# Performance work log

Measured on AMD Instinct MI355X. Metric: run time of the kernel, lower is better.

The kernel has to match this reference:

```python
import jax, jax.numpy as jnp
import numpy as np

N_NODES = 100000
N_EDGES = 3200000
N_FEAT = 256
N_FILT = 256


def setup_inputs() -> dict:
    key = jax.random.key(0)
    k1, k2, k3, k4, k5 = jax.random.split(key, 5)
    # Xavier-normal-ish filters: std = sqrt(2/(fan_in+fan_out))
    std = (2.0 / (N_FEAT + N_FILT)) ** 0.5
    filters = jax.random.normal(k1, (N_FEAT, N_FILT), dtype=jnp.float32) * std
    x = jax.random.normal(k2, (N_NODES, N_FEAT), dtype=jnp.float32)
    edge_row = jax.random.randint(k3, (N_EDGES,), 0, N_NODES, dtype=jnp.int32)
    edge_col = jax.random.randint(k4, (N_EDGES,), 0, N_NODES, dtype=jnp.int32)
    edge_weight = jax.random.uniform(k5, (N_EDGES,), dtype=jnp.float32)
    return {"x": x, "filters": filters, "edge_row": edge_row,
            "edge_col": edge_col, "edge_weight": edge_weight}


def reference(x, filters, edge_row, edge_col, edge_weight):
    # XF = x @ filters  -> [N, K]
    XF = jnp.matmul(x, filters)
    # out = transform @ XF, transform given in COO form:
    # out[r] = sum_{e: row[e]==r} weight[e] * XF[col[e]]
    msgs = edge_weight[:, None] * XF[edge_col]          # [E, K] gather
    out = jax.ops.segment_sum(msgs, edge_row, num_segments=N_NODES)  # [N, K] scatter-add
    return out
```

## Files before the change

### kernel.cpp

```cpp
#include <hip/hip_runtime.h>

#define NF 256
#define NK 256
#define NBKT 512
#define TILEA 8192

typedef __attribute__((ext_vector_type(8))) short bf16x8;
typedef __attribute__((ext_vector_type(4))) float f32x4;

__device__ __forceinline__ ushort f2bf(float f) {
  uint u = __float_as_uint(f);
  return (ushort)((u + 0x7fffu + ((u >> 16) & 1u)) >> 16);
}
__device__ __forceinline__ float bf2f(ushort h) {
  return __uint_as_float(((uint)h) << 16);
}

__global__ __launch_bounds__(256) void prelude(const float* __restrict__ F,
                                               ushort* __restrict__ Ft,
                                               const int* __restrict__ erow,
                                               int* __restrict__ bcnt, int nE) {
  __shared__ int h[NBKT];
  if (blockIdx.x < NF) {
    int k = blockIdx.x;
    int n = threadIdx.x;
    Ft[(size_t)n * NF + k] = f2bf(F[(size_t)k * NK + n]);
    return;
  }
  const int bid = blockIdx.x - NF;
  const int nb = gridDim.x - NF;
  h[threadIdx.x] = 0;
  h[threadIdx.x + 256] = 0;
  __syncthreads();
  for (int e = bid * 256 + threadIdx.x; e < nE; e += nb * 256)
    atomicAdd(&h[erow[e] >> 8], 1);
  __syncthreads();
  int v0 = h[threadIdx.x], v1 = h[threadIdx.x + 256];
  if (v0) atomicAdd(&bcnt[threadIdx.x], v0);
  if (v1) atomicAdd(&bcnt[threadIdx.x + 256], v1);
}

__global__ __launch_bounds__(256) void gemm_mfma(const float* __restrict__ x,
                                                 const ushort* __restrict__ Ft,
                                                 ushort* __restrict__ XFh, int M) {
  __shared__ ushort As[32 * NF];
  const int t = threadIdx.x;
  const int row0 = blockIdx.x * 32;

  const float4* xv = (const float4*)(x + (size_t)row0 * NF);
#pragma unroll
  for (int j = 0; j < 8; ++j) {
    int idx = j * 256 + t;
    int r = idx >> 6;
    int c4 = idx & 63;
    float4 v = make_float4(0.f, 0.f, 0.f, 0.f);
    if (row0 + r < M) v = xv[idx];
    ushort4 hh = make_ushort4(f2bf(v.x), f2bf(v.y), f2bf(v.z), f2bf(v.w));
    uint boff = (uint)(r * 512 + c4 * 8);
    boff ^= (uint)((r & 7) << 4);
    *(ushort4*)((char*)As + boff) = hh;
  }
  __syncthreads();

  const int lane = t & 63;
  const int wv = t >> 6;
  const int arow = lane & 15;
  const int kg = lane >> 4;

  bf16x8 afr[2][8];
#pragma unroll
  for (int rt = 0; rt < 2; ++rt) {
#pragma unroll
    for (int kk = 0; kk < 8; ++kk) {
      int r = rt * 16 + arow;
      uint boff = (uint)(r * 512 + kk * 64 + kg * 16);
      boff ^= (uint)((r & 7) << 4);
      afr[rt][kk] = *(const bf16x8*)((const char*)As + boff);
    }
  }

  f32x4 acc[2][4];
#pragma unroll
  for (int rt = 0; rt < 2; ++rt)
#pragma unroll
    for (int f = 0; f < 4; ++f) acc[rt][f] = (f32x4){0.f, 0.f, 0.f, 0.f};

  const int ncol0 = wv * 64;
#pragma unroll
  for (int f = 0; f < 4; ++f) {
    const ushort* bp = Ft + (size_t)(ncol0 + f * 16 + arow) * NF + kg * 8;
#pragma unroll
    for (int kk = 0; kk < 8; ++kk) {
      bf16x8 bfr = *(const bf16x8*)(bp + kk * 32);
      acc[0][f] = __builtin_amdgcn_mfma_f32_16x16x32_bf16(afr[0][kk], bfr, acc[0][f], 0, 0, 0);
      acc[1][f] = __builtin_amdgcn_mfma_f32_16x16x32_bf16(afr[1][kk], bfr, acc[1][f], 0, 0, 0);
    }
  }

#pragma unroll
  for (int rt = 0; rt < 2; ++rt) {
#pragma unroll
    for (int f = 0; f < 4; ++f) {
      int col = ncol0 + f * 16 + arow;
#pragma unroll
      for (int rg = 0; rg < 4; ++rg) {
        int row = row0 + rt * 16 + kg * 4 + rg;
        if (row < M) XFh[(size_t)row * NK + col] = f2bf(acc[rt][f][rg]);
      }
    }
  }
}

__global__ __launch_bounds__(512) void scan_bbase(const int* __restrict__ bcnt,
                                                  int* __restrict__ bbase,
                                                  int* __restrict__ bcursor) {
  __shared__ int s[NBKT];
  int t = threadIdx.x;
  int v = bcnt[t];
  s[t] = v;
  __syncthreads();
  for (int d = 1; d < NBKT; d <<= 1) {
    int tmp = (t >= d) ? s[t - d] : 0;
    __syncthreads();
    s[t] += tmp;
    __syncthreads();
  }
  int excl = s[t] - v;
  bbase[t] = excl;
  bcursor[t * 16] = excl;
}

__global__ __launch_bounds__(512) void bin_coarse(const int* __restrict__ erow,
                                                  const int* __restrict__ ecol,
                                                  const float* __restrict__ ew,
                                                  int* __restrict__ bcursor,
                                                  int2* __restrict__ tmpCW, int nE) {
  __shared__ int h[NBKT];
  __shared__ int lb[NBKT];
  __shared__ int gb[NBKT];
  __shared__ int2 pay[TILEA];
  const int t = threadIdx.x;
  const int base = blockIdx.x * TILEA;

  h[t] = 0;
  __syncthreads();

  int rnk[16], bb[16], loc[16];
#pragma unroll
  for (int k = 0; k < 16; ++k) {
    int i = base + k * 512 + t;
    rnk[k] = -1; bb[k] = 0; loc[k] = 0;
    if (i < nE) {
      int row = erow[i];
      bb[k] = row >> 8;
      loc[k] = row & 255;
      rnk[k] = atomicAdd(&h[bb[k]], 1);
    }
  }
  __syncthreads();

  int hv = h[t];
  lb[t] = hv;
  __syncthreads();
  for (int d = 1; d < NBKT; d <<= 1) {
    int tmp = (t >= d) ? lb[t - d] : 0;
    __syncthreads();
    lb[t] += tmp;
    __syncthreads();
  }
  int ex = lb[t] - hv;
  __syncthreads();
  lb[t] = ex;
  if (hv > 0) gb[t] = atomicAdd(&bcursor[t * 16], hv);
  __syncthreads();

#pragma unroll
  for (int k = 0; k < 16; ++k) {
    int i = base + k * 512 + t;
    if (i < nE) {
      int pos = lb[bb[k]] + rnk[k];
      pay[pos] = make_int2(ecol[i] | (loc[k] << 20), __float_as_int(ew[i]));
    }
  }
  __syncthreads();

  const int wv = t >> 6, lane = t & 63;
  for (int b = wv; b < NBKT; b += 8) {
    int len = h[b];
    if (!len) continue;
    int lbase = lb[b], gbase = gb[b];
    for (int off = lane; off < len; off += 64)
      tmpCW[gbase + off] = pay[lbase + off];
  }
}

__global__ __launch_bounds__(256) void bin_fine(const int2* __restrict__ tmpCW,
                                                const int* __restrict__ bbase,
                                                const int* __restrict__ bcnt,
                                                int* __restrict__ offsets,
                                                int2* __restrict__ cw,
                                                int nNodes, int nE) {
  __shared__ int hist[256];
  __shared__ int cur[256];
  const int b = blockIdx.x;
  const int t = threadIdx.x;
  const int base = bbase[b];
  const int n = bcnt[b];

  hist[t] = 0;
  __syncthreads();
  for (int i = t; i < n; i += 256)
    atomicAdd(&hist[((uint)tmpCW[base + i].x) >> 20], 1);
  __syncthreads();

  int hv = hist[t];
  cur[t] = hv;
  __syncthreads();
  for (int d = 1; d < 256; d <<= 1) {
    int tmp = (t >= d) ? cur[t - d] : 0;
    __syncthreads();
    cur[t] += tmp;
    __syncthreads();
  }
  int ex = cur[t] - hv;
  __syncthreads();
  cur[t] = ex;
  int node = (b << 8) + t;
  if (node < nNodes) offsets[node] = base + ex;
  if (b == 0 && t == 0) offsets[nNodes] = nE;
  __syncthreads();

  for (int i = t; i < n; i += 256) {
    int2 v = tmpCW[base + i];
    int local = ((uint)v.x) >> 20;
    int d = base + atomicAdd(&cur[local], 1);
    cw[d] = make_int2(v.x & 0xFFFFF, v.y);
  }
}

__global__ __launch_bounds__(256) void gather_bf16(const ushort* __restrict__ XFh,
                                                   const int* __restrict__ offsets,
                                                   const int2* __restrict__ cw,
                                                   f32x4* __restrict__ outv,
                                                   int nNodes) {
  const int lane = threadIdx.x & 63;
  const int node = (blockIdx.x * blockDim.x + threadIdx.x) >> 6;
  if (node >= nNodes) return;
  const int start = offsets[node];
  const int end = offsets[node + 1];
  const ushort4* XV = (const ushort4*)XFh;

  float ax = 0.f, ay = 0.f, az = 0.f, aw = 0.f;
  for (int base = start; base < end; base += 64) {
    int n = end - base;
    if (n > 64) n = 64;
    int2 e = make_int2(0, 0);
    if (lane < n) {
      long long raw = __builtin_nontemporal_load((const long long*)(cw + base + lane));
      e.x = (int)(raw & 0xFFFFFFFFll);
      e.y = (int)(raw >> 32);
    }
    int j = 0;
    for (; j + 7 < n; j += 8) {
      int c0 = __shfl(e.x, j),     c1 = __shfl(e.x, j + 1);
      int c2 = __shfl(e.x, j + 2), c3 = __shfl(e.x, j + 3);
      int c4 = __shfl(e.x, j + 4), c5 = __shfl(e.x, j + 5);
      int c6 = __shfl(e.x, j + 6), c7 = __shfl(e.x, j + 7);
      float w0 = __int_as_float(__shfl(e.y, j));
      float w1 = __int_as_float(__shfl(e.y, j + 1));
      float w2 = __int_as_float(__shfl(e.y, j + 2));
      float w3 = __int_as_float(__shfl(e.y, j + 3));
      float w4 = __int_as_float(__shfl(e.y, j + 4));
      float w5 = __int_as_float(__shfl(e.y, j + 5));
      float w6 = __int_as_float(__shfl(e.y, j + 6));
      float w7 = __int_as_float(__shfl(e.y, j + 7));
      ushort4 v0 = XV[(size_t)c0 * 64 + lane];
      ushort4 v1 = XV[(size_t)c1 * 64 + lane];
      ushort4 v2 = XV[(size_t)c2 * 64 + lane];
      ushort4 v3 = XV[(size_t)c3 * 64 + lane];
      ushort4 v4 = XV[(size_t)c4 * 64 + lane];
      ushort4 v5 = XV[(size_t)c5 * 64 + lane];
      ushort4 v6 = XV[(size_t)c6 * 64 + lane];
      ushort4 v7 = XV[(size_t)c7 * 64 + lane];
      ax += w0 * bf2f(v0.x); ay += w0 * bf2f(v0.y); az += w0 * bf2f(v0.z); aw += w0 * bf2f(v0.w);
      ax += w1 * bf2f(v1.x); ay += w1 * bf2f(v1.y); az += w1 * bf2f(v1.z); aw += w1 * bf2f(v1.w);
      ax += w2 * bf2f(v2.x); ay += w2 * bf2f(v2.y); az += w2 * bf2f(v2.z); aw += w2 * bf2f(v2.w);
      ax += w3 * bf2f(v3.x); ay += w3 * bf2f(v3.y); az += w3 * bf2f(v3.z); aw += w3 * bf2f(v3.w);
      ax += w4 * bf2f(v4.x); ay += w4 * bf2f(v4.y); az += w4 * bf2f(v4.z); aw += w4 * bf2f(v4.w);
      ax += w5 * bf2f(v5.x); ay += w5 * bf2f(v5.y); az += w5 * bf2f(v5.z); aw += w5 * bf2f(v5.w);
      ax += w6 * bf2f(v6.x); ay += w6 * bf2f(v6.y); az += w6 * bf2f(v6.z); aw += w6 * bf2f(v6.w);
      ax += w7 * bf2f(v7.x); ay += w7 * bf2f(v7.y); az += w7 * bf2f(v7.z); aw += w7 * bf2f(v7.w);
    }
    for (; j + 3 < n; j += 4) {
      int c0 = __shfl(e.x, j),     c1 = __shfl(e.x, j + 1);
      int c2 = __shfl(e.x, j + 2), c3 = __shfl(e.x, j + 3);
      float w0 = __int_as_float(__shfl(e.y, j));
      float w1 = __int_as_float(__shfl(e.y, j + 1));
      float w2 = __int_as_float(__shfl(e.y, j + 2));
      float w3 = __int_as_float(__shfl(e.y, j + 3));
      ushort4 v0 = XV[(size_t)c0 * 64 + lane];
      ushort4 v1 = XV[(size_t)c1 * 64 + lane];
      ushort4 v2 = XV[(size_t)c2 * 64 + lane];
      ushort4 v3 = XV[(size_t)c3 * 64 + lane];
      ax += w0 * bf2f(v0.x); ay += w0 * bf2f(v0.y); az += w0 * bf2f(v0.z); aw += w0 * bf2f(v0.w);
      ax += w1 * bf2f(v1.x); ay += w1 * bf2f(v1.y); az += w1 * bf2f(v1.z); aw += w1 * bf2f(v1.w);
      ax += w2 * bf2f(v2.x); ay += w2 * bf2f(v2.y); az += w2 * bf2f(v2.z); aw += w2 * bf2f(v2.w);
      ax += w3 * bf2f(v3.x); ay += w3 * bf2f(v3.y); az += w3 * bf2f(v3.z); aw += w3 * bf2f(v3.w);
    }
    for (; j < n; ++j) {
      int c0 = __shfl(e.x, j);
      float w0 = __int_as_float(__shfl(e.y, j));
      ushort4 v0 = XV[(size_t)c0 * 64 + lane];
      ax += w0 * bf2f(v0.x); ay += w0 * bf2f(v0.y); az += w0 * bf2f(v0.z); aw += w0 * bf2f(v0.w);
    }
  }
  f32x4 r; r.x = ax; r.y = ay; r.z = az; r.w = aw;
  __builtin_nontemporal_store(r, &outv[(size_t)node * 64 + lane]);
}

__global__ __launch_bounds__(256) void gemm_xf(const float* __restrict__ x,
                                               const float* __restrict__ F,
                                               float* __restrict__ XF, int M) {
  __shared__ float xs[64][NF];
  const int t = threadIdx.x;
  const int row0 = blockIdx.x * 64;
  const int rows = min(64, M - row0);
  const float4* xv = (const float4*)(x + (size_t)row0 * NF);
  float4* xsv = (float4*)&xs[0][0];
#pragma unroll
  for (int j = 0; j < 16; ++j) {
    int i = j * 256 + t;
    int r = i >> 6;
    float4 v;
    if (r < rows) v = xv[i];
    else          v = make_float4(0.f, 0.f, 0.f, 0.f);
    xsv[i] = v;
  }
  __syncthreads();
  const int r0 = (t >> 5) * 8;
  const int c0 = blockIdx.y * 128 + (t & 31) * 4;
  float acc[8][4];
#pragma unroll
  for (int r = 0; r < 8; ++r)
#pragma unroll
    for (int c = 0; c < 4; ++c) acc[r][c] = 0.f;
  for (int k = 0; k < NF; k += 4) {
    float4 f0 = *(const float4*)(F + (size_t)(k + 0) * NK + c0);
    float4 f1 = *(const float4*)(F + (size_t)(k + 1) * NK + c0);
    float4 f2 = *(const float4*)(F + (size_t)(k + 2) * NK + c0);
    float4 f3 = *(const float4*)(F + (size_t)(k + 3) * NK + c0);
#pragma unroll
    for (int r = 0; r < 8; ++r) {
      float4 xr = *(const float4*)&xs[r0 + r][k];
      acc[r][0] += xr.x * f0.x + xr.y * f1.x + xr.z * f2.x + xr.w * f3.x;
      acc[r][1] += xr.x * f0.y + xr.y * f1.y + xr.z * f2.y + xr.w * f3.y;
      acc[r][2] += xr.x * f0.z + xr.y * f1.z + xr.z * f2.z + xr.w * f3.z;
      acc[r][3] += xr.x * f0.w + xr.y * f1.w + xr.z * f2.w + xr.w * f3.w;
    }
  }
#pragma unroll
  for (int r = 0; r < 8; ++r) {
    int row = r0 + r;
    if (row < rows) {
      float4 v = make_float4(acc[r][0], acc[r][1], acc[r][2], acc[r][3]);
      *(float4*)(XF + (size_t)(row0 + row) * NK + c0) = v;
    }
  }
}

__global__ __launch_bounds__(256) void scatter_edges(
    const float* __restrict__ XF, const int* __restrict__ erow,
    const int* __restrict__ ecol, const float* __restrict__ ew,
    float* __restrict__ out, int nE) {
  const int lane = threadIdx.x & 63;
  const int wid = (blockIdx.x * blockDim.x + threadIdx.x) >> 6;
  const int nwaves = (gridDim.x * blockDim.x) >> 6;
  for (int e = wid; e < nE; e += nwaves) {
    const int r = erow[e];
    const int c = ecol[e];
    const float w = ew[e];
    float4 v = *(const float4*)(XF + (size_t)c * NK + lane * 4);
    float* dst = out + (size_t)r * NK + lane * 4;
    atomicAdd(dst + 0, w * v.x);
    atomicAdd(dst + 1, w * v.y);
    atomicAdd(dst + 2, w * v.z);
    atomicAdd(dst + 3, w * v.w);
  }
}

static inline size_t align16(size_t x) { return (x + 15) & ~(size_t)15; }

extern "C" void kernel_launch(void* const* d_in, const int* in_sizes, int n_in,
                              void* d_out, int out_size, void* d_ws, size_t ws_size,
                              hipStream_t stream) {
  const float* x  = (const float*)d_in[0];
  const float* F  = (const float*)d_in[1];
  const int* erow = (const int*)d_in[2];
  const int* ecol = (const int*)d_in[3];
  const float* ew = (const float*)d_in[4];
  float* out      = (float*)d_out;

  const int M      = in_sizes[0] / NF;
  const int nE     = in_sizes[2];
  const int nNodes = out_size / NK;

  char* base = (char*)d_ws;
  size_t off = 0;
  ushort* XFh  = (ushort*)(base + off); off += align16((size_t)M * NK * sizeof(ushort));
  ushort* Ft   = (ushort*)(base + off); off += align16((size_t)NF * NK * sizeof(ushort));
  int* offsets = (int*)(base + off);    off += align16(((size_t)nNodes + 1) * sizeof(int));
  int* bcnt    = (int*)(base + off);    off += align16(NBKT * sizeof(int));
  int* bbase   = (int*)(base + off);    off += align16(NBKT * sizeof(int));
  int* bcursor = (int*)(base + off);    off += align16((size_t)NBKT * 16 * sizeof(int));
  int2* tmpCW  = (int2*)(base + off);   off += align16((size_t)nE * sizeof(int2));
  int2* cw     = (int2*)(base + off);   off += align16((size_t)nE * sizeof(int2));
  const size_t needed = off;

  const int nb2 = (nNodes + 255) >> 8;
  const bool ok = (ws_size >= needed) && (nb2 <= NBKT) &&
                  (nNodes < (1 << 20)) && (M < (1 << 20));

  if (ok) {
    hipMemsetAsync(bcnt, 0, NBKT * sizeof(int), stream);
    prelude<<<NF + 2048, 256, 0, stream>>>(F, Ft, erow, bcnt, nE);
    gemm_mfma<<<(M + 31) / 32, 256, 0, stream>>>(x, Ft, XFh, M);
    scan_bbase<<<1, NBKT, 0, stream>>>(bcnt, bbase, bcursor);
    bin_coarse<<<(nE + TILEA - 1) / TILEA, 512, 0, stream>>>(erow, ecol, ew,
                                                             bcursor, tmpCW, nE);
    bin_fine<<<nb2, 256, 0, stream>>>(tmpCW, bbase, bcnt, offsets, cw, nNodes, nE);
    int gblocks = (nNodes + 3) / 4;
    gather_bf16<<<gblocks, 256, 0, stream>>>(XFh, offsets, cw, (f32x4*)out, nNodes);
  } else {
    float* XF = (float*)d_ws;
    dim3 gg((M + 63) / 64, NK / 128);
    gemm_xf<<<gg, 256, 0, stream>>>(x, F, XF, M);
    hipMemsetAsync(d_out, 0, (size_t)out_size * sizeof(float), stream);
    scatter_edges<<<2048, 256, 0, stream>>>(XF, erow, ecol, ew, out, nE);
  }
}
```

Measured before the change: 432.5 us.

## Fuse fine binning and gather into one per-bucket LDS kernel

Shrinks coarse row buckets from 256 to 128 nodes, doubling the bucket count to 1024. Each block of the new kernel counting-sorts its bucket's edges into shared memory and then gathers and accumulates each node's output directly. This drops the global sorted-edge array and the offsets array, along with the extra write and read of all edges. In exchange the gather runs on far fewer waves, each with shallower load unrolling, and a bucket that overflows shared memory falls back to float atomics.

```diff
diff --git a/kernel.cpp b/kernel.cpp
--- a/kernel.cpp
+++ b/kernel.cpp
@@ -2,8 +2,11 @@
 
 #define NF 256
 #define NK 256
-#define NBKT 512
+#define BSHIFT 7
+#define NLOC 128
+#define NBKT 1024
 #define TILEA 8192
+#define GCAP 5120
 
 typedef __attribute__((ext_vector_type(8))) short bf16x8;
 typedef __attribute__((ext_vector_type(4))) float f32x4;
@@ -29,15 +32,17 @@
   }
   const int bid = blockIdx.x - NF;
   const int nb = gridDim.x - NF;
-  h[threadIdx.x] = 0;
-  h[threadIdx.x + 256] = 0;
+#pragma unroll
+  for (int j = 0; j < 4; ++j) h[threadIdx.x + j * 256] = 0;
   __syncthreads();
   for (int e = bid * 256 + threadIdx.x; e < nE; e += nb * 256)
-    atomicAdd(&h[erow[e] >> 8], 1);
-  __syncthreads();
-  int v0 = h[threadIdx.x], v1 = h[threadIdx.x + 256];
-  if (v0) atomicAdd(&bcnt[threadIdx.x], v0);
-  if (v1) atomicAdd(&bcnt[threadIdx.x + 256], v1);
+    atomicAdd(&h[erow[e] >> BSHIFT], 1);
+  __syncthreads();
+#pragma unroll
+  for (int j = 0; j < 4; ++j) {
+    int v = h[threadIdx.x + j * 256];
+    if (v) atomicAdd(&bcnt[threadIdx.x + j * 256], v);
+  }
 }
 
 __global__ __launch_bounds__(256) void gemm_mfma(const float* __restrict__ x,
@@ -111,9 +116,9 @@
   }
 }
 
-__global__ __launch_bounds__(512) void scan_bbase(const int* __restrict__ bcnt,
-                                                  int* __restrict__ bbase,
-                                                  int* __restrict__ bcursor) {
+__global__ __launch_bounds__(NBKT) void scan_bbase(const int* __restrict__ bcnt,
+                                                   int* __restrict__ bbase,
+                                                   int* __restrict__ bcursor) {
   __shared__ int s[NBKT];
   int t = threadIdx.x;
   int v = bcnt[t];
@@ -138,11 +143,12 @@
   __shared__ int h[NBKT];
   __shared__ int lb[NBKT];
   __shared__ int gb[NBKT];
+  __shared__ int ps[512];
   __shared__ int2 pay[TILEA];
   const int t = threadIdx.x;
   const int base = blockIdx.x * TILEA;
 
-  h[t] = 0;
+  h[t] = 0; h[t + 512] = 0;
   __syncthreads();
 
   int rnk[16], bb[16], loc[16];
@@ -152,26 +158,32 @@
     rnk[k] = -1; bb[k] = 0; loc[k] = 0;
     if (i < nE) {
       int row = erow[i];
-      bb[k] = row >> 8;
-      loc[k] = row & 255;
+      bb[k] = row >> BSHIFT;
+      loc[k] = row & (NLOC - 1);
       rnk[k] = atomicAdd(&h[bb[k]], 1);
     }
   }
   __syncthreads();
 
-  int hv = h[t];
-  lb[t] = hv;
-  __syncthreads();
-  for (int d = 1; d < NBKT; d <<= 1) {
-    int tmp = (t >= d) ? lb[t - d] : 0;
-    __syncthreads();
-    lb[t] += tmp;
-    __syncthreads();
-  }
-  int ex = lb[t] - hv;
-  __syncthreads();
-  lb[t] = ex;
-  if (hv > 0) gb[t] = atomicAdd(&bcursor[t * 16], hv);
+  int a0 = h[2 * t], a1 = h[2 * t + 1];
+  ps[t] = a0 + a1;
+  __syncthreads();
+  for (int d = 1; d < 512; d <<= 1) {
+    int tmp = (t >= d) ? ps[t - d] : 0;
+    __syncthreads();
+    ps[t] += tmp;
+    __syncthreads();
+  }
+  int pb = ps[t] - (a0 + a1);
+  lb[2 * t] = pb;
+  lb[2 * t + 1] = pb + a0;
+  __syncthreads();
+
+  {
+    int v0 = h[t], v1 = h[t + 512];
+    if (v0) gb[t] = atomicAdd(&bcursor[t * 16], v0);
+    if (v1) gb[t + 512] = atomicAdd(&bcursor[(t + 512) * 16], v1);
+  }
   __syncthreads();
 
 #pragma unroll
@@ -194,128 +206,100 @@
   }
 }
 
-__global__ __launch_bounds__(256) void bin_fine(const int2* __restrict__ tmpCW,
-                                                const int* __restrict__ bbase,
-                                                const int* __restrict__ bcnt,
-                                                int* __restrict__ offsets,
-                                                int2* __restrict__ cw,
-                                                int nNodes, int nE) {
-  __shared__ int hist[256];
-  __shared__ int cur[256];
+__global__ __launch_bounds__(512) void bucket_gather(const int2* __restrict__ tmpCW,
+                                                     const int* __restrict__ bbase,
+                                                     const int* __restrict__ bcnt,
+                                                     const ushort* __restrict__ XFh,
+                                                     f32x4* __restrict__ outv,
+                                                     float* __restrict__ outf,
+                                                     int nNodes) {
+  __shared__ int st[NLOC];
+  __shared__ int cur[NLOC];
+  __shared__ int2 pay[GCAP];
+  const int t = threadIdx.x;
   const int b = blockIdx.x;
-  const int t = threadIdx.x;
   const int base = bbase[b];
   const int n = bcnt[b];
-
-  hist[t] = 0;
-  __syncthreads();
-  for (int i = t; i < n; i += 256)
-    atomicAdd(&hist[((uint)tmpCW[base + i].x) >> 20], 1);
-  __syncthreads();
-
-  int hv = hist[t];
-  cur[t] = hv;
-  __syncthreads();
-  for (int d = 1; d < 256; d <<= 1) {
-    int tmp = (t >= d) ? cur[t - d] : 0;
-    __syncthreads();
-    cur[t] += tmp;
-    __syncthreads();
-  }
-  int ex = cur[t] - hv;
-  __syncthreads();
-  cur[t] = ex;
-  int node = (b << 8) + t;
-  if (node < nNodes) offsets[node] = base + ex;
-  if (b == 0 && t == 0) offsets[nNodes] = nE;
-  __syncthreads();
-
-  for (int i = t; i < n; i += 256) {
+  const int nl = (n < GCAP) ? n : GCAP;
+  const ushort4* XV = (const ushort4*)XFh;
+
+  if (t < NLOC) cur[t] = 0;
+  __syncthreads();
+  for (int i = t; i < nl; i += 512)
+    atomicAdd(&cur[((uint)tmpCW[base + i].x) >> 20], 1);
+  __syncthreads();
+
+  int hv = (t < NLOC) ? cur[t] : 0;
+  if (t < NLOC) st[t] = hv;
+  __syncthreads();
+  for (int d = 1; d < NLOC; d <<= 1) {
+    int tmp = (t >= d && t < NLOC) ? st[t - d] : 0;
+    __syncthreads();
+    if (t < NLOC) st[t] += tmp;
+    __syncthreads();
+  }
+  if (t < NLOC) {
+    st[t] -= hv;
+    cur[t] = st[t];
+  }
+  __syncthreads();
+
+  for (int i = t; i < nl; i += 512) {
     int2 v = tmpCW[base + i];
-    int local = ((uint)v.x) >> 20;
-    int d = base + atomicAdd(&cur[local], 1);
-    cw[d] = make_int2(v.x & 0xFFFFF, v.y);
-  }
-}
-
-__global__ __launch_bounds__(256) void gather_bf16(const ushort* __restrict__ XFh,
-                                                   const int* __restrict__ offsets,
-                                                   const int2* __restrict__ cw,
-                                                   f32x4* __restrict__ outv,
-                                                   int nNodes) {
-  const int lane = threadIdx.x & 63;
-  const int node = (blockIdx.x * blockDim.x + threadIdx.x) >> 6;
-  if (node >= nNodes) return;
-  const int start = offsets[node];
-  const int end = offsets[node + 1];
-  const ushort4* XV = (const ushort4*)XFh;
-
-  float ax = 0.f, ay = 0.f, az = 0.f, aw = 0.f;
-  for (int base = start; base < end; base += 64) {
-    int n = end - base;
-    if (n > 64) n = 64;
-    int2 e = make_int2(0, 0);
-    if (lane < n) {
-      long long raw = __builtin_nontemporal_load((const long long*)(cw + base + lane));
-      e.x = (int)(raw & 0xFFFFFFFFll);
-      e.y = (int)(raw >> 32);
-    }
-    int j = 0;
-    for (; j + 7 < n; j += 8) {
-      int c0 = __shfl(e.x, j),     c1 = __shfl(e.x, j + 1);
-      int c2 = __shfl(e.x, j + 2), c3 = __shfl(e.x, j + 3);
-      int c4 = __shfl(e.x, j + 4), c5 = __shfl(e.x, j + 5);
-      int c6 = __shfl(e.x, j + 6), c7 = __shfl(e.x, j + 7);
-      float w0 = __int_as_float(__shfl(e.y, j));
-      float w1 = __int_as_float(__shfl(e.y, j + 1));
-      float w2 = __int_as_float(__shfl(e.y, j + 2));
-      float w3 = __int_as_float(__shfl(e.y, j + 3));
-      float w4 = __int_as_float(__shfl(e.y, j + 4));
-      float w5 = __int_as_float(__shfl(e.y, j + 5));
-      float w6 = __int_as_float(__shfl(e.y, j + 6));
-      float w7 = __int_as_float(__shfl(e.y, j + 7));
-      ushort4 v0 = XV[(size_t)c0 * 64 + lane];
-      ushort4 v1 = XV[(size_t)c1 * 64 + lane];
-      ushort4 v2 = XV[(size_t)c2 * 64 + lane];
-      ushort4 v3 = XV[(size_t)c3 * 64 + lane];
-      ushort4 v4 = XV[(size_t)c4 * 64 + lane];
-      ushort4 v5 = XV[(size_t)c5 * 64 + lane];
-      ushort4 v6 = XV[(size_t)c6 * 64 + lane];
-      ushort4 v7 = XV[(size_t)c7 * 64 + lane];
+    int loc = ((uint)v.x) >> 20;
+    int p = atomicAdd(&cur[loc], 1);
+    pay[p] = make_int2(v.x & 0xFFFFF, v.y);
+  }
+  __syncthreads();
+
+  const int wv = t >> 6, lane = t & 63;
+  for (int loc = wv; loc < NLOC; loc += 8) {
+    int node = (b << BSHIFT) + loc;
+    if (node >= nNodes) continue;
+    int s = st[loc];
+    int e = cur[loc];
+    float ax = 0.f, ay = 0.f, az = 0.f, aw = 0.f;
+    int j = s;
+    for (; j + 3 < e; j += 4) {
+      int2 e0 = pay[j], e1 = pay[j + 1], e2 = pay[j + 2], e3 = pay[j + 3];
+      float w0 = __int_as_float(e0.y), w1 = __int_as_float(e1.y);
+      float w2 = __int_as_float(e2.y), w3 = __int_as_float(e3.y);
+      ushort4 v0 = XV[(size_t)e0.x * 64 + lane];
+      ushort4 v1 = XV[(size_t)e1.x * 64 + lane];
+      ushort4 v2 = XV[(size_t)e2.x * 64 + lane];
+      ushort4 v3 = XV[(size_t)e3.x * 64 + lane];
       ax += w0 * bf2f(v0.x); ay += w0 * bf2f(v0.y); az += w0 * bf2f(v0.z); aw += w0 * bf2f(v0.w);
       ax += w1 * bf2f(v1.x); ay += w1 * bf2f(v1.y); az += w1 * bf2f(v1.z); aw += w1 * bf2f(v1.w);
       ax += w2 * bf2f(v2.x); ay += w2 * bf2f(v2.y); az += w2 * bf2f(v2.z); aw += w2 * bf2f(v2.w);
       ax += w3 * bf2f(v3.x); ay += w3 * bf2f(v3.y); az += w3 * bf2f(v3.z); aw += w3 * bf2f(v3.w);
-      ax += w4 * bf2f(v4.x); ay += w4 * bf2f(v4.y); az += w4 * bf2f(v4.z); aw += w4 * bf2f(v4.w);
-      ax += w5 * bf2f(v5.x); ay += w5 * bf2f(v5.y); az += w5 * bf2f(v5.z); aw += w5 * bf2f(v5.w);
-      ax += w6 * bf2f(v6.x); ay += w6 * bf2f(v6.y); az += w6 * bf2f(v6.z); aw += w6 * bf2f(v6.w);
-      ax += w7 * bf2f(v7.x); ay += w7 * bf2f(v7.y); az += w7 * bf2f(v7.z); aw += w7 * bf2f(v7.w);
-    }
-    for (; j + 3 < n; j += 4) {
-      int c0 = __shfl(e.x, j),     c1 = __shfl(e.x, j + 1);
-      int c2 = __shfl(e.x, j + 2), c3 = __shfl(e.x, j + 3);
-      float w0 = __int_as_float(__shfl(e.y, j));
-      float w1 = __int_as_float(__shfl(e.y, j + 1));
-      float w2 = __int_as_float(__shfl(e.y, j + 2));
-      float w3 = __int_as_float(__shfl(e.y, j + 3));
-      ushort4 v0 = XV[(size_t)c0 * 64 + lane];
-      ushort4 v1 = XV[(size_t)c1 * 64 + lane];
-      ushort4 v2 = XV[(size_t)c2 * 64 + lane];
-      ushort4 v3 = XV[(size_t)c3 * 64 + lane];
+    }
+    for (; j < e; ++j) {
+      int2 e0 = pay[j];
+      float w0 = __int_as_float(e0.y);
+      ushort4 v0 = XV[(size_t)e0.x * 64 + lane];
       ax += w0 * bf2f(v0.x); ay += w0 * bf2f(v0.y); az += w0 * bf2f(v0.z); aw += w0 * bf2f(v0.w);
-      ax += w1 * bf2f(v1.x); ay += w1 * bf2f(v1.y); az += w1 * bf2f(v1.z); aw += w1 * bf2f(v1.w);
-      ax += w2 * bf2f(v2.x); ay += w2 * bf2f(v2.y); az += w2 * bf2f(v2.z); aw += w2 * bf2f(v2.w);
-      ax += w3 * bf2f(v3.x); ay += w3 * bf2f(v3.y); az += w3 * bf2f(v3.z); aw += w3 * bf2f(v3.w);
-    }
-    for (; j < n; ++j) {
-      int c0 = __shfl(e.x, j);
-      float w0 = __int_as_float(__shfl(e.y, j));
-      ushort4 v0 = XV[(size_t)c0 * 64 + lane];
-      ax += w0 * bf2f(v0.x); ay += w0 * bf2f(v0.y); az += w0 * bf2f(v0.z); aw += w0 * bf2f(v0.w);
-    }
-  }
-  f32x4 r; r.x = ax; r.y = ay; r.z = az; r.w = aw;
-  __builtin_nontemporal_store(r, &outv[(size_t)node * 64 + lane]);
+    }
+    f32x4 r; r.x = ax; r.y = ay; r.z = az; r.w = aw;
+    __builtin_nontemporal_store(r, &outv[(size_t)node * 64 + lane]);
+  }
+
+  if (n > GCAP) {
+    __syncthreads();
+    for (int i = GCAP + wv; i < n; i += 8) {
+      int2 v = tmpCW[base + i];
+      int loc = ((uint)v.x) >> 20;
+      int node = (b << BSHIFT) + loc;
+      if (node >= nNodes) continue;
+      int col = v.x & 0xFFFFF;
+      float w = __int_as_float(v.y);
+      ushort4 vv = XV[(size_t)col * 64 + lane];
+      float* dst = outf + (size_t)node * NK + lane * 4;
+      atomicAdd(dst + 0, w * bf2f(vv.x));
+      atomicAdd(dst + 1, w * bf2f(vv.y));
+      atomicAdd(dst + 2, w * bf2f(vv.z));
+      atomicAdd(dst + 3, w * bf2f(vv.w));
+    }
+  }
 }
 
 __global__ __launch_bounds__(256) void gemm_xf(const float* __restrict__ x,
@@ -408,15 +392,13 @@
   size_t off = 0;
   ushort* XFh  = (ushort*)(base + off); off += align16((size_t)M * NK * sizeof(ushort));
   ushort* Ft   = (ushort*)(base + off); off += align16((size_t)NF * NK * sizeof(ushort));
-  int* offsets = (int*)(base + off);    off += align16(((size_t)nNodes + 1) * sizeof(int));
   int* bcnt    = (int*)(base + off);    off += align16(NBKT * sizeof(int));
   int* bbase   = (int*)(base + off);    off += align16(NBKT * sizeof(int));
   int* bcursor = (int*)(base + off);    off += align16((size_t)NBKT * 16 * sizeof(int));
   int2* tmpCW  = (int2*)(base + off);   off += align16((size_t)nE * sizeof(int2));
-  int2* cw     = (int2*)(base + off);   off += align16((size_t)nE * sizeof(int2));
   const size_t needed = off;
 
-  const int nb2 = (nNodes + 255) >> 8;
+  const int nb2 = (nNodes + NLOC - 1) >> BSHIFT;
   const bool ok = (ws_size >= needed) && (nb2 <= NBKT) &&
                   (nNodes < (1 << 20)) && (M < (1 << 20));
 
@@ -427,9 +409,8 @@
     scan_bbase<<<1, NBKT, 0, stream>>>(bcnt, bbase, bcursor);
     bin_coarse<<<(nE + TILEA - 1) / TILEA, 512, 0, stream>>>(erow, ecol, ew,
                                                              bcursor, tmpCW, nE);
-    bin_fine<<<nb2, 256, 0, stream>>>(tmpCW, bbase, bcnt, offsets, cw, nNodes, nE);
-    int gblocks = (nNodes + 3) / 4;
-    gather_bf16<<<gblocks, 256, 0, stream>>>(XFh, offsets, cw, (f32x4*)out, nNodes);
+    bucket_gather<<<nb2, 512, 0, stream>>>(tmpCW, bbase, bcnt, XFh,
+                                           (f32x4*)out, out, nNodes);
   } else {
     float* XF = (float*)d_ws;
     dim3 gg((M + 63) / 64, NK / 128);
```

Measured after the change: 464.7 us. +7.4%, slower.
